# Kernel tuning notes

Hardware: AMD Instinct MI355X
Metric: run time of the kernel (lower is better)

## Reference

```python
import jax, jax.numpy as jnp
import numpy as np

B, T, D, H = 4, 2048, 512, 8
K = D // H  # head dim = 64

def setup_inputs() -> dict:
    key = jax.random.key(0)
    k1, k2, k3, k4 = jax.random.split(key, 4)
    x = jax.random.normal(k1, (B, T, D), dtype=jnp.float32)
    # torch nn.Linear stores weight as [out_features, in_features]
    w_qkv = jax.random.normal(k2, (3 * D, D), dtype=jnp.float32) * (D ** -0.5)
    w_proj = jax.random.normal(k3, (D, D), dtype=jnp.float32) * (D ** -0.5)
    b_proj = jax.random.normal(k4, (D,), dtype=jnp.float32) * 0.01
    return {"x": x, "w_qkv": w_qkv, "w_proj": w_proj, "b_proj": b_proj}

def reference(x, w_qkv, w_proj, b_proj):
    Bx, Tx, Dx = x.shape
    # qkv projection (no bias): [B,T,3D]
    qkv = jnp.einsum('btd,ed->bte', x, w_qkv)
    q, k, v = jnp.split(qkv, 3, axis=-1)
    # [B,H,T,K]
    def heads(t):
        return t.reshape(Bx, Tx, H, K).transpose(0, 2, 1, 3)
    q, k, v = heads(q), heads(k), heads(v)
    # scaled scores with causal mask
    scores = jnp.einsum('bhqk,bhsk->bhqs', q, k) * (K ** -0.5)  # [B,H,T,T]
    causal = jnp.tril(jnp.ones((Tx, Tx), dtype=bool))
    scores = jnp.where(causal, scores, -jnp.inf)
    attn = jax.nn.softmax(scores, axis=-1)  # dropout p=0.0 -> identity
    out = jnp.einsum('bhqs,bhsk->bhqk', attn, v)  # [B,H,T,K]
    out = out.transpose(0, 2, 1, 3).reshape(Bx, Tx, Dx)
    out = jnp.einsum('btd,ed->bte', out, w_proj) + b_proj
    return out
```

## Files before the change

kernel.cpp:

```cpp
#include <hip/hip_runtime.h>


typedef unsigned short u16;
typedef __attribute__((ext_vector_type(8))) __bf16 bf16x8;
typedef __attribute__((ext_vector_type(8))) unsigned short u16x8;
typedef __attribute__((ext_vector_type(4))) float f32x4;

#define DEV static __device__ __forceinline__

DEV void async16(const u16* g, u16* l) {
  __builtin_amdgcn_global_load_lds(
      (const __attribute__((address_space(1))) unsigned int*)g,
      (__attribute__((address_space(3))) unsigned int*)l, 16, 0, 0);
}
DEV u16x8 gld8(const u16* p) { return *(const u16x8*)p; }
DEV void lst8(u16* p, u16x8 v) { *(u16x8*)p = v; }
DEV bf16x8 ldsld8(const u16* p) {
  return __builtin_bit_cast(bf16x8, *(const u16x8*)p);
}
DEV f32x4 mfma16(bf16x8 a, bf16x8 b, f32x4 c) {
  return __builtin_amdgcn_mfma_f32_16x16x32_bf16(a, b, c, 0, 0, 0);
}
DEV u16 f2b(float f) {
  unsigned u = __builtin_bit_cast(unsigned, f);
  u += 0x7FFFu + ((u >> 16) & 1u);
  return (u16)(u >> 16);
}
DEV u16x8 pack8(f32x4 a, f32x4 b) {
  u16x8 r;
  r[0] = f2b(a[0]); r[1] = f2b(a[1]); r[2] = f2b(a[2]); r[3] = f2b(a[3]);
  r[4] = f2b(b[0]); r[5] = f2b(b[1]); r[6] = f2b(b[2]); r[7] = f2b(b[3]);
  return r;
}

__global__ void cvt_all(const float* __restrict__ x, const float* __restrict__ wq,
                        u16* __restrict__ xb, u16* __restrict__ wqb) {
  constexpr long NX = 8192L * 512 / 8;
  constexpr long NQ = 1536L * 512 / 8;
  const long i = (long)blockIdx.x * 256 + threadIdx.x;
  if (i < NX) {
    const float* p = x + i * 8;
    *(u16x8*)(xb + i * 8) = pack8(*(const f32x4*)p, *(const f32x4*)(p + 4));
  } else if (i < NX + NQ) {
    const long j = i - NX;
    const float* p = wq + j * 8;
    *(u16x8*)(wqb + j * 8) = pack8(*(const f32x4*)p, *(const f32x4*)(p + 4));
  }
}

__global__ void gemm_bb(const u16* __restrict__ A, const u16* __restrict__ Bt,
                        u16* __restrict__ C, int N, int K) {
  __shared__ __align__(16) u16 As[2][128 * 32];
  __shared__ __align__(16) u16 Bs[2][128 * 32];

  const int t = threadIdx.x, lane = t & 63, w = t >> 6;
  const int lane15 = lane & 15, quad = lane >> 4;
  const int wr = w >> 1, wc = w & 1;
  const long row0 = (long)blockIdx.y * 128;
  const int col0 = blockIdx.x * 128;

  const int srow = w * 16 + (lane >> 2);
  const int scol = (lane & 3) * 8;
  const u16* Ag = A + (row0 + srow) * (long)K + scol;
  const u16* Bg = Bt + ((long)col0 + srow) * (long)K + scol;

  f32x4 acc[4][4];
#pragma unroll
  for (int i = 0; i < 4; i++)
#pragma unroll
    for (int j = 0; j < 4; j++) acc[i][j] = (f32x4)(0.0f);

  for (int k0 = 0; k0 < K; k0 += 64) {
    __syncthreads();
#pragma unroll
    for (int r = 0; r < 2; r++) {
#pragma unroll
      for (int hf = 0; hf < 2; hf++) {
        async16(Ag + (long)r * 64 * K + k0 + hf * 32,
                &As[hf][(r * 64 + w * 16) * 32]);
        async16(Bg + (long)r * 64 * K + k0 + hf * 32,
                &Bs[hf][(r * 64 + w * 16) * 32]);
      }
    }
    __syncthreads();

#pragma unroll
    for (int hf = 0; hf < 2; hf++) {
      bf16x8 a[4], b[4];
#pragma unroll
      for (int i = 0; i < 4; i++)
        a[i] = ldsld8(&As[hf][(wr * 64 + i * 16 + lane15) * 32 + quad * 8]);
#pragma unroll
      for (int j = 0; j < 4; j++)
        b[j] = ldsld8(&Bs[hf][(wc * 64 + j * 16 + lane15) * 32 + quad * 8]);
#pragma unroll
      for (int i = 0; i < 4; i++)
#pragma unroll
        for (int j = 0; j < 4; j++) acc[i][j] = mfma16(a[i], b[j], acc[i][j]);
    }
  }

#pragma unroll
  for (int i = 0; i < 4; i++)
#pragma unroll
    for (int j = 0; j < 4; j++) {
      const int col = col0 + wc * 64 + j * 16 + lane15;
#pragma unroll
      for (int r = 0; r < 4; r++) {
        const long row = row0 + wr * 64 + i * 16 + quad * 4 + r;
        C[row * (long)N + col] = f2b(acc[i][j][r]);
      }
    }
}

__global__ void gemm_b64(const u16* __restrict__ A, const float* __restrict__ Bt,
                         const float* __restrict__ bias, float* __restrict__ C,
                         int N, int K) {
  __shared__ __align__(16) u16 As[2][128 * 32];
  __shared__ __align__(16) u16 Bs[2][64 * 32];

  const int t = threadIdx.x, lane = t & 63, w = t >> 6;
  const int lane15 = lane & 15, quad = lane >> 4;
  const int wr = w >> 1, wc = w & 1;
  const long row0 = (long)blockIdx.y * 128;
  const int col0 = blockIdx.x * 64;

  const int srow = w * 16 + (lane >> 2);
  const int scol = (lane & 3) * 8;
  const u16* Ag = A + (row0 + srow) * (long)K + scol;

  const int brow = t >> 2, bc = (t & 3) * 16;
  const float* Bg = Bt + (long)(col0 + brow) * K + bc;
  u16* BsD = &Bs[bc >> 5][brow * 32 + (bc & 31)];

  f32x4 acc[4][2];
#pragma unroll
  for (int i = 0; i < 4; i++)
#pragma unroll
    for (int j = 0; j < 2; j++) acc[i][j] = (f32x4)(0.0f);

  f32x4 q0 = *(const f32x4*)Bg, q1 = *(const f32x4*)(Bg + 4);
  f32x4 q2 = *(const f32x4*)(Bg + 8), q3 = *(const f32x4*)(Bg + 12);

  for (int k0 = 0; k0 < K; k0 += 64) {
    __syncthreads();
#pragma unroll
    for (int r = 0; r < 2; r++)
#pragma unroll
      for (int hf = 0; hf < 2; hf++)
        async16(Ag + (long)r * 64 * K + k0 + hf * 32,
                &As[hf][(r * 64 + w * 16) * 32]);
    lst8(BsD, pack8(q0, q1));
    lst8(BsD + 8, pack8(q2, q3));
    __syncthreads();

    {
      const int kp = (k0 + 64 < K) ? k0 + 64 : k0;
      q0 = *(const f32x4*)(Bg + kp);     q1 = *(const f32x4*)(Bg + kp + 4);
      q2 = *(const f32x4*)(Bg + kp + 8); q3 = *(const f32x4*)(Bg + kp + 12);
    }

#pragma unroll
    for (int hf = 0; hf < 2; hf++) {
      bf16x8 a[4], b[2];
#pragma unroll
      for (int i = 0; i < 4; i++)
        a[i] = ldsld8(&As[hf][(wr * 64 + i * 16 + lane15) * 32 + quad * 8]);
#pragma unroll
      for (int j = 0; j < 2; j++)
        b[j] = ldsld8(&Bs[hf][(wc * 32 + j * 16 + lane15) * 32 + quad * 8]);
#pragma unroll
      for (int i = 0; i < 4; i++)
#pragma unroll
        for (int j = 0; j < 2; j++) acc[i][j] = mfma16(a[i], b[j], acc[i][j]);
    }
  }

#pragma unroll
  for (int i = 0; i < 4; i++)
#pragma unroll
    for (int j = 0; j < 2; j++) {
      const int col = col0 + wc * 32 + j * 16 + lane15;
      const float bv = bias[col];
#pragma unroll
      for (int r = 0; r < 4; r++) {
        const long row = row0 + wr * 64 + i * 16 + quad * 4 + r;
        C[row * (long)N + col] = acc[i][j][r] + bv;
      }
    }
}

__global__ void attn_v3(const u16* __restrict__ qkv, u16* __restrict__ out) {
  constexpr int T = 2048, LD = 1536;
  constexpr float CEXP = 0.18033688f;
  __shared__ __align__(16) u16 Ks[64 * 72];
  __shared__ __align__(16) u16 Vt[64 * 72];
  __shared__ __align__(16) u16 Ps[4][16 * 72];

  const int t = threadIdx.x, lane = t & 63, w = t >> 6;
  const int lane15 = lane & 15, quad = lane >> 4;

  const int i = blockIdx.x;
  int qb = i & 31;
  if (i >= 512) qb = 31 - qb;
  const int h = (i >> 5) & 7;
  const int b = (i >> 8) & 3;
  const long base = (long)b * T * LD;

  const u16* gq =
      qkv + base + (long)(qb * 64 + w * 16 + lane15) * LD + h * 64 + quad * 8;
  const bf16x8 qa0 = __builtin_bit_cast(bf16x8, *(const u16x8*)gq);
  const bf16x8 qa1 = __builtin_bit_cast(bf16x8, *(const u16x8*)(gq + 32));

  const int srow = t >> 3, sc8 = (t & 7) * 8;
  const int vs = t >> 2, vd0 = (t & 3) * 16;

  const int nsb = qb + 1;

  u16x8 kr0, kr1, vr0, vr1;
  {
    const u16* gk = qkv + base + (long)srow * LD + 512 + h * 64 + sc8;
    const u16* gv = qkv + base + (long)vs * LD + 1024 + h * 64 + vd0;
    kr0 = gld8(gk); kr1 = gld8(gk + (long)32 * LD);
    vr0 = gld8(gv); vr1 = gld8(gv + 8);
  }

  float lp[4] = {0.0f, 0.0f, 0.0f, 0.0f};
  f32x4 o[4];
#pragma unroll
  for (int j = 0; j < 4; j++) o[j] = (f32x4)(0.0f);

  const int qrow_base = qb * 64 + w * 16 + quad * 4;

  for (int sb = 0; sb < nsb; ++sb) {
    __syncthreads();
    lst8(&Ks[srow * 72 + sc8], kr0);
    lst8(&Ks[(srow + 32) * 72 + sc8], kr1);
#pragma unroll
    for (int ii = 0; ii < 8; ii++) {
      const int d = vd0 + ii;
      Vt[d * 72 + (vs ^ (((d >> 3) & 7) << 3))] = vr0[ii];
    }
#pragma unroll
    for (int ii = 0; ii < 8; ii++) {
      const int d = vd0 + 8 + ii;
      Vt[d * 72 + (vs ^ (((d >> 3) & 7) << 3))] = vr1[ii];
    }
    __syncthreads();

    {
      const int sp = (sb + 1 < nsb) ? sb + 1 : sb;
      const u16* gk = qkv + base + (long)(sp * 64 + srow) * LD + 512 + h * 64 + sc8;
      const u16* gv = qkv + base + (long)(sp * 64 + vs) * LD + 1024 + h * 64 + vd0;
      kr0 = gld8(gk); kr1 = gld8(gk + (long)32 * LD);
      vr0 = gld8(gv); vr1 = gld8(gv + 8);
    }

    f32x4 sf[4];
#pragma unroll
    for (int j = 0; j < 4; j++) {
      f32x4 z = (f32x4)(0.0f);
      z = mfma16(qa0, ldsld8(&Ks[(j * 16 + lane15) * 72 + quad * 8]), z);
      sf[j] = mfma16(qa1, ldsld8(&Ks[(j * 16 + lane15) * 72 + quad * 8 + 32]), z);
    }

    if (sb == qb) {
      const int scol_base = sb * 64 + lane15;
#pragma unroll
      for (int j = 0; j < 4; j++)
#pragma unroll
        for (int r = 0; r < 4; r++) {
          float p = exp2f(sf[j][r] * CEXP);
          if (scol_base + j * 16 > qrow_base + r) p = 0.0f;
          sf[j][r] = p;
          lp[r] += p;
        }
    } else {
#pragma unroll
      for (int j = 0; j < 4; j++)
#pragma unroll
        for (int r = 0; r < 4; r++) {
          const float p = exp2f(sf[j][r] * CEXP);
          sf[j][r] = p;
          lp[r] += p;
        }
    }

    u16* myP = Ps[w];
#pragma unroll
    for (int j = 0; j < 4; j++)
#pragma unroll
      for (int r = 0; r < 4; r++)
        myP[(quad * 4 + r) * 72 + j * 16 + lane15] = f2b(sf[j][r]);
    __asm__ __volatile__("" ::: "memory");
    const bf16x8 pa0 = ldsld8(&myP[lane15 * 72 + quad * 8]);
    const bf16x8 pa1 = ldsld8(&myP[lane15 * 72 + quad * 8 + 32]);
    __asm__ __volatile__("" ::: "memory");

#pragma unroll
    for (int j = 0; j < 4; j++) {
      const int d0 = j * 16 + lane15;
      const int swz = ((d0 >> 3) & 7) << 3;
      o[j] = mfma16(pa0, ldsld8(&Vt[d0 * 72 + ((quad * 8) ^ swz)]), o[j]);
      o[j] = mfma16(pa1, ldsld8(&Vt[d0 * 72 + ((quad * 8 + 32) ^ swz)]), o[j]);
    }
  }

#pragma unroll
  for (int off = 1; off < 16; off <<= 1)
#pragma unroll
    for (int r = 0; r < 4; r++) lp[r] += __shfl_xor(lp[r], off);

  const long orow0 = (long)b * T + qb * 64 + w * 16;
  float inv[4];
#pragma unroll
  for (int r = 0; r < 4; r++) inv[r] = 1.0f / lp[r];
#pragma unroll
  for (int j = 0; j < 4; j++)
#pragma unroll
    for (int r = 0; r < 4; r++)
      out[(orow0 + quad * 4 + r) * 512 + h * 64 + j * 16 + lane15] =
          f2b(o[j][r] * inv[r]);
}

extern "C" void kernel_launch(void* const* d_in, const int* in_sizes, int n_in,
                              void* d_out, int out_size, void* d_ws, size_t ws_size,
                              hipStream_t stream) {
  const float* x      = (const float*)d_in[0];
  const float* w_qkv  = (const float*)d_in[1];
  const float* w_proj = (const float*)d_in[2];
  const float* b_proj = (const float*)d_in[3];
  float* out = (float*)d_out;

  u16* qkv = (u16*)d_ws;
  u16* xb  = qkv + (size_t)8192 * 1536;
  u16* wqb = (u16*)d_out;

  cvt_all<<<2432, 256, 0, stream>>>(x, w_qkv, xb, wqb);
  gemm_bb<<<dim3(12, 64), 256, 0, stream>>>(xb, wqb, qkv, 1536, 512);
  attn_v3<<<1024, 256, 0, stream>>>(qkv, xb);
  gemm_b64<<<dim3(8, 64), 256, 0, stream>>>(xb, w_proj, b_proj, out, 512, 512);
}
```

Baseline: 163.8 us.

## Fuse fp32-to-bf16 conversion into QKV GEMM and enlarge attention query tiles

Removes the separate conversion kernel: the QKV GEMM now loads fp32 x and weights, packs them to bf16 in registers and stores to LDS, with register prefetch of the next K tile instead of async global-to-LDS loads. The attention kernel moves to 512-thread blocks covering 128 query rows (8 waves) sharing each K/V tile, which halves K/V loads per query, and waves skip key blocks that lie fully above their causal range. Bf16 packing switches to the HIP intrinsic conversion. The costs are more fp32 global traffic inside the GEMM, synchronous loads in place of the async path, and idle waves at block barriers on the diagonal.

```diff
diff --git a/kernel.cpp b/kernel.cpp
--- a/kernel.cpp
+++ b/kernel.cpp
@@ -1,10 +1,12 @@
 #include <hip/hip_runtime.h>
+#include <hip/hip_bf16.h>
 
 
 typedef unsigned short u16;
 typedef __attribute__((ext_vector_type(8))) __bf16 bf16x8;
 typedef __attribute__((ext_vector_type(8))) unsigned short u16x8;
 typedef __attribute__((ext_vector_type(4))) float f32x4;
+typedef __attribute__((ext_vector_type(4))) unsigned u32x4;
 
 #define DEV static __device__ __forceinline__
 
@@ -26,30 +28,23 @@
   u += 0x7FFFu + ((u >> 16) & 1u);
   return (u16)(u >> 16);
 }
+DEV unsigned pk2(float x, float y) {
+  __hip_bfloat162 t = __float22bfloat162_rn(float2{x, y});
+  unsigned r;
+  __builtin_memcpy(&r, &t, 4);
+  return r;
+}
 DEV u16x8 pack8(f32x4 a, f32x4 b) {
-  u16x8 r;
-  r[0] = f2b(a[0]); r[1] = f2b(a[1]); r[2] = f2b(a[2]); r[3] = f2b(a[3]);
-  r[4] = f2b(b[0]); r[5] = f2b(b[1]); r[6] = f2b(b[2]); r[7] = f2b(b[3]);
-  return r;
-}
-
-__global__ void cvt_all(const float* __restrict__ x, const float* __restrict__ wq,
-                        u16* __restrict__ xb, u16* __restrict__ wqb) {
-  constexpr long NX = 8192L * 512 / 8;
-  constexpr long NQ = 1536L * 512 / 8;
-  const long i = (long)blockIdx.x * 256 + threadIdx.x;
-  if (i < NX) {
-    const float* p = x + i * 8;
-    *(u16x8*)(xb + i * 8) = pack8(*(const f32x4*)p, *(const f32x4*)(p + 4));
-  } else if (i < NX + NQ) {
-    const long j = i - NX;
-    const float* p = wq + j * 8;
-    *(u16x8*)(wqb + j * 8) = pack8(*(const f32x4*)p, *(const f32x4*)(p + 4));
-  }
-}
-
-__global__ void gemm_bb(const u16* __restrict__ A, const u16* __restrict__ Bt,
-                        u16* __restrict__ C, int N, int K) {
+  u32x4 t;
+  t[0] = pk2(a[0], a[1]);
+  t[1] = pk2(a[2], a[3]);
+  t[2] = pk2(b[0], b[1]);
+  t[3] = pk2(b[2], b[3]);
+  return __builtin_bit_cast(u16x8, t);
+}
+
+__global__ void gemm1f(const float* __restrict__ A, const float* __restrict__ Bt,
+                       u16* __restrict__ C, int N, int K) {
   __shared__ __align__(16) u16 As[2][128 * 32];
   __shared__ __align__(16) u16 Bs[2][128 * 32];
 
@@ -59,10 +54,18 @@
   const long row0 = (long)blockIdx.y * 128;
   const int col0 = blockIdx.x * 128;
 
-  const int srow = w * 16 + (lane >> 2);
-  const int scol = (lane & 3) * 8;
-  const u16* Ag = A + (row0 + srow) * (long)K + scol;
-  const u16* Bg = Bt + ((long)col0 + srow) * (long)K + scol;
+  const int sr = t >> 2, sc = (t & 3) * 8;
+  const float* Ag = A + (row0 + sr) * (long)K + sc;
+  const float* Bg = Bt + (long)(col0 + sr) * K + sc;
+  u16* AsD[2][2];
+  u16* BsD[2][2];
+#pragma unroll
+  for (int r = 0; r < 2; r++)
+#pragma unroll
+    for (int hf = 0; hf < 2; hf++) {
+      AsD[r][hf] = &As[hf][(sr + r * 64) * 32 + sc];
+      BsD[r][hf] = &Bs[hf][(sr + r * 64) * 32 + sc];
+    }
 
   f32x4 acc[4][4];
 #pragma unroll
@@ -70,19 +73,40 @@
 #pragma unroll
     for (int j = 0; j < 4; j++) acc[i][j] = (f32x4)(0.0f);
 
+  u16x8 ra[2][2], rb[2][2];
+#pragma unroll
+  for (int r = 0; r < 2; r++)
+#pragma unroll
+    for (int hf = 0; hf < 2; hf++) {
+      const float* pa = Ag + (long)r * 64 * K + hf * 32;
+      const float* pb = Bg + (long)r * 64 * K + hf * 32;
+      ra[r][hf] = pack8(*(const f32x4*)pa, *(const f32x4*)(pa + 4));
+      rb[r][hf] = pack8(*(const f32x4*)pb, *(const f32x4*)(pb + 4));
+    }
+
   for (int k0 = 0; k0 < K; k0 += 64) {
     __syncthreads();
 #pragma unroll
-    for (int r = 0; r < 2; r++) {
+    for (int r = 0; r < 2; r++)
 #pragma unroll
       for (int hf = 0; hf < 2; hf++) {
-        async16(Ag + (long)r * 64 * K + k0 + hf * 32,
-                &As[hf][(r * 64 + w * 16) * 32]);
-        async16(Bg + (long)r * 64 * K + k0 + hf * 32,
-                &Bs[hf][(r * 64 + w * 16) * 32]);
+        lst8(AsD[r][hf], ra[r][hf]);
+        lst8(BsD[r][hf], rb[r][hf]);
       }
-    }
-    __syncthreads();
+    __syncthreads();
+
+    {
+      const int kp = (k0 + 64 < K) ? k0 + 64 : k0;
+#pragma unroll
+      for (int r = 0; r < 2; r++)
+#pragma unroll
+        for (int hf = 0; hf < 2; hf++) {
+          const float* pa = Ag + (long)r * 64 * K + kp + hf * 32;
+          const float* pb = Bg + (long)r * 64 * K + kp + hf * 32;
+          ra[r][hf] = pack8(*(const f32x4*)pa, *(const f32x4*)(pa + 4));
+          rb[r][hf] = pack8(*(const f32x4*)pb, *(const f32x4*)(pb + 4));
+        }
+    }
 
 #pragma unroll
     for (int hf = 0; hf < 2; hf++) {
@@ -190,39 +214,39 @@
     }
 }
 
-__global__ void attn_v3(const u16* __restrict__ qkv, u16* __restrict__ out) {
+__global__ void attn_v4(const u16* __restrict__ qkv, u16* __restrict__ out) {
   constexpr int T = 2048, LD = 1536;
   constexpr float CEXP = 0.18033688f;
   __shared__ __align__(16) u16 Ks[64 * 72];
   __shared__ __align__(16) u16 Vt[64 * 72];
-  __shared__ __align__(16) u16 Ps[4][16 * 72];
+  __shared__ __align__(16) u16 Ps[8][16 * 72];
 
   const int t = threadIdx.x, lane = t & 63, w = t >> 6;
   const int lane15 = lane & 15, quad = lane >> 4;
 
   const int i = blockIdx.x;
-  int qb = i & 31;
-  if (i >= 512) qb = 31 - qb;
-  const int h = (i >> 5) & 7;
-  const int b = (i >> 8) & 3;
+  int qt = i & 15;
+  if (i >= 256) qt = 15 - qt;
+  const int h = (i >> 4) & 7;
+  const int b = (i >> 7) & 3;
   const long base = (long)b * T * LD;
 
   const u16* gq =
-      qkv + base + (long)(qb * 64 + w * 16 + lane15) * LD + h * 64 + quad * 8;
+      qkv + base + (long)(qt * 128 + w * 16 + lane15) * LD + h * 64 + quad * 8;
   const bf16x8 qa0 = __builtin_bit_cast(bf16x8, *(const u16x8*)gq);
   const bf16x8 qa1 = __builtin_bit_cast(bf16x8, *(const u16x8*)(gq + 32));
 
   const int srow = t >> 3, sc8 = (t & 7) * 8;
-  const int vs = t >> 2, vd0 = (t & 3) * 16;
-
-  const int nsb = qb + 1;
-
-  u16x8 kr0, kr1, vr0, vr1;
+  const int vs = t >> 3, vd0 = (t & 7) * 8;
+
+  const int nsb = 2 * qt + 2;
+
+  u16x8 kr, vr;
   {
     const u16* gk = qkv + base + (long)srow * LD + 512 + h * 64 + sc8;
     const u16* gv = qkv + base + (long)vs * LD + 1024 + h * 64 + vd0;
-    kr0 = gld8(gk); kr1 = gld8(gk + (long)32 * LD);
-    vr0 = gld8(gv); vr1 = gld8(gv + 8);
+    kr = gld8(gk);
+    vr = gld8(gv);
   }
 
   float lp[4] = {0.0f, 0.0f, 0.0f, 0.0f};
@@ -230,21 +254,16 @@
 #pragma unroll
   for (int j = 0; j < 4; j++) o[j] = (f32x4)(0.0f);
 
-  const int qrow_base = qb * 64 + w * 16 + quad * 4;
+  const int qrow_base = qt * 128 + w * 16 + quad * 4;
+  const int qrow_wave_max = qt * 128 + w * 16 + 15;
 
   for (int sb = 0; sb < nsb; ++sb) {
     __syncthreads();
-    lst8(&Ks[srow * 72 + sc8], kr0);
-    lst8(&Ks[(srow + 32) * 72 + sc8], kr1);
+    lst8(&Ks[srow * 72 + sc8], kr);
 #pragma unroll
     for (int ii = 0; ii < 8; ii++) {
       const int d = vd0 + ii;
-      Vt[d * 72 + (vs ^ (((d >> 3) & 7) << 3))] = vr0[ii];
-    }
-#pragma unroll
-    for (int ii = 0; ii < 8; ii++) {
-      const int d = vd0 + 8 + ii;
-      Vt[d * 72 + (vs ^ (((d >> 3) & 7) << 3))] = vr1[ii];
+      Vt[d * 72 + (vs ^ (((d >> 3) & 7) << 3))] = vr[ii];
     }
     __syncthreads();
 
@@ -252,9 +271,11 @@
       const int sp = (sb + 1 < nsb) ? sb + 1 : sb;
       const u16* gk = qkv + base + (long)(sp * 64 + srow) * LD + 512 + h * 64 + sc8;
       const u16* gv = qkv + base + (long)(sp * 64 + vs) * LD + 1024 + h * 64 + vd0;
-      kr0 = gld8(gk); kr1 = gld8(gk + (long)32 * LD);
-      vr0 = gld8(gv); vr1 = gld8(gv + 8);
-    }
+      kr = gld8(gk);
+      vr = gld8(gv);
+    }
+
+    if (sb * 64 > qrow_wave_max) continue;
 
     f32x4 sf[4];
 #pragma unroll
@@ -264,7 +285,7 @@
       sf[j] = mfma16(qa1, ldsld8(&Ks[(j * 16 + lane15) * 72 + quad * 8 + 32]), z);
     }
 
-    if (sb == qb) {
+    if (sb >= 2 * qt) {
       const int scol_base = sb * 64 + lane15;
 #pragma unroll
       for (int j = 0; j < 4; j++)
@@ -311,7 +332,7 @@
 #pragma unroll
     for (int r = 0; r < 4; r++) lp[r] += __shfl_xor(lp[r], off);
 
-  const long orow0 = (long)b * T + qb * 64 + w * 16;
+  const long orow0 = (long)b * T + qt * 128 + w * 16;
   float inv[4];
 #pragma unroll
   for (int r = 0; r < 4; r++) inv[r] = 1.0f / lp[r];
@@ -332,12 +353,10 @@
   const float* b_proj = (const float*)d_in[3];
   float* out = (float*)d_out;
 
-  u16* qkv = (u16*)d_ws;
-  u16* xb  = qkv + (size_t)8192 * 1536;
-  u16* wqb = (u16*)d_out;
-
-  cvt_all<<<2432, 256, 0, stream>>>(x, w_qkv, xb, wqb);
-  gemm_bb<<<dim3(12, 64), 256, 0, stream>>>(xb, wqb, qkv, 1536, 512);
-  attn_v3<<<1024, 256, 0, stream>>>(qkv, xb);
-  gemm_b64<<<dim3(8, 64), 256, 0, stream>>>(xb, w_proj, b_proj, out, 512, 512);
-}
+  u16* qkv  = (u16*)d_ws;
+  u16* attn = qkv + (size_t)8192 * 1536;
+
+  gemm1f<<<dim3(12, 64), 256, 0, stream>>>(x, w_qkv, qkv, 1536, 512);
+  attn_v4<<<512, 512, 0, stream>>>(qkv, attn);
+  gemm_b64<<<dim3(8, 64), 256, 0, stream>>>(attn, w_proj, b_proj, out, 512, 512);
+}
```

After: 232.8 us. +42.1%, slower.

## Process two query sub-tiles per attention block to share K/V staging

Applied to the files above, without the earlier changes.

The attention kernel now handles 128 query rows per block, split into two 64-row sub-tiles, so each K/V tile staged into LDS serves both. This halves the number of blocks and the global K/V reads, with heavy tiles scheduled first. The softmax scale is folded into the Q columns in the QKV GEMM epilogue, which removes a multiply inside the exp loop. The bf16 packing now uses the packed HIP conversion intrinsic. In exchange, each block holds more registers and the grid is half as large, which may lower occupancy and load balance.

```diff
diff --git a/kernel.cpp b/kernel.cpp
--- a/kernel.cpp
+++ b/kernel.cpp
@@ -1,10 +1,12 @@
 #include <hip/hip_runtime.h>
+#include <hip/hip_bf16.h>
 
 
 typedef unsigned short u16;
 typedef __attribute__((ext_vector_type(8))) __bf16 bf16x8;
 typedef __attribute__((ext_vector_type(8))) unsigned short u16x8;
 typedef __attribute__((ext_vector_type(4))) float f32x4;
+typedef __attribute__((ext_vector_type(4))) unsigned u32x4;
 
 #define DEV static __device__ __forceinline__
 
@@ -26,11 +28,19 @@
   u += 0x7FFFu + ((u >> 16) & 1u);
   return (u16)(u >> 16);
 }
+DEV unsigned pk2(float x, float y) {
+  __hip_bfloat162 t = __float22bfloat162_rn(float2{x, y});
+  unsigned r;
+  __builtin_memcpy(&r, &t, 4);
+  return r;
+}
 DEV u16x8 pack8(f32x4 a, f32x4 b) {
-  u16x8 r;
-  r[0] = f2b(a[0]); r[1] = f2b(a[1]); r[2] = f2b(a[2]); r[3] = f2b(a[3]);
-  r[4] = f2b(b[0]); r[5] = f2b(b[1]); r[6] = f2b(b[2]); r[7] = f2b(b[3]);
-  return r;
+  u32x4 t;
+  t[0] = pk2(a[0], a[1]);
+  t[1] = pk2(a[2], a[3]);
+  t[2] = pk2(b[0], b[1]);
+  t[3] = pk2(b[2], b[3]);
+  return __builtin_bit_cast(u16x8, t);
 }
 
 __global__ void cvt_all(const float* __restrict__ x, const float* __restrict__ wq,
@@ -73,7 +83,7 @@
   for (int k0 = 0; k0 < K; k0 += 64) {
     __syncthreads();
 #pragma unroll
-    for (int r = 0; r < 2; r++) {
+    for (int r = 0; r < 2; r++)
 #pragma unroll
       for (int hf = 0; hf < 2; hf++) {
         async16(Ag + (long)r * 64 * K + k0 + hf * 32,
@@ -81,7 +91,6 @@
         async16(Bg + (long)r * 64 * K + k0 + hf * 32,
                 &Bs[hf][(r * 64 + w * 16) * 32]);
       }
-    }
     __syncthreads();
 
 #pragma unroll
@@ -105,10 +114,11 @@
 #pragma unroll
     for (int j = 0; j < 4; j++) {
       const int col = col0 + wc * 64 + j * 16 + lane15;
+      const float sc = (col < 512) ? 0.18033688f : 1.0f;
 #pragma unroll
       for (int r = 0; r < 4; r++) {
         const long row = row0 + wr * 64 + i * 16 + quad * 4 + r;
-        C[row * (long)N + col] = f2b(acc[i][j][r]);
+        C[row * (long)N + col] = f2b(acc[i][j][r] * sc);
       }
     }
 }
@@ -190,32 +200,34 @@
     }
 }
 
-__global__ void attn_v3(const u16* __restrict__ qkv, u16* __restrict__ out) {
+__global__ void attn_v5(const u16* __restrict__ qkv, u16* __restrict__ out) {
   constexpr int T = 2048, LD = 1536;
-  constexpr float CEXP = 0.18033688f;
   __shared__ __align__(16) u16 Ks[64 * 72];
   __shared__ __align__(16) u16 Vt[64 * 72];
-  __shared__ __align__(16) u16 Ps[4][16 * 72];
+  __shared__ __align__(16) u16 Ps[4][2][16 * 72];
 
   const int t = threadIdx.x, lane = t & 63, w = t >> 6;
   const int lane15 = lane & 15, quad = lane >> 4;
 
-  const int i = blockIdx.x;
-  int qb = i & 31;
-  if (i >= 512) qb = 31 - qb;
-  const int h = (i >> 5) & 7;
-  const int b = (i >> 8) & 3;
+  const int bx = blockIdx.x;
+  const int qt = 15 - (bx >> 5);
+  const int h = bx & 7, b = (bx >> 3) & 3;
   const long base = (long)b * T * LD;
 
-  const u16* gq =
-      qkv + base + (long)(qb * 64 + w * 16 + lane15) * LD + h * 64 + quad * 8;
-  const bf16x8 qa0 = __builtin_bit_cast(bf16x8, *(const u16x8*)gq);
-  const bf16x8 qa1 = __builtin_bit_cast(bf16x8, *(const u16x8*)(gq + 32));
+  bf16x8 qa[2][2];
+#pragma unroll
+  for (int sp = 0; sp < 2; sp++) {
+    const u16* gq = qkv + base +
+                    (long)(qt * 128 + sp * 64 + w * 16 + lane15) * LD +
+                    h * 64 + quad * 8;
+    qa[sp][0] = __builtin_bit_cast(bf16x8, *(const u16x8*)gq);
+    qa[sp][1] = __builtin_bit_cast(bf16x8, *(const u16x8*)(gq + 32));
+  }
 
   const int srow = t >> 3, sc8 = (t & 7) * 8;
   const int vs = t >> 2, vd0 = (t & 3) * 16;
 
-  const int nsb = qb + 1;
+  const int nsb = 2 * qt + 2;
 
   u16x8 kr0, kr1, vr0, vr1;
   {
@@ -225,12 +237,12 @@
     vr0 = gld8(gv); vr1 = gld8(gv + 8);
   }
 
-  float lp[4] = {0.0f, 0.0f, 0.0f, 0.0f};
-  f32x4 o[4];
-#pragma unroll
-  for (int j = 0; j < 4; j++) o[j] = (f32x4)(0.0f);
-
-  const int qrow_base = qb * 64 + w * 16 + quad * 4;
+  float lp[2][4] = {{0, 0, 0, 0}, {0, 0, 0, 0}};
+  f32x4 o[2][4];
+#pragma unroll
+  for (int sp = 0; sp < 2; sp++)
+#pragma unroll
+    for (int j = 0; j < 4; j++) o[sp][j] = (f32x4)(0.0f);
 
   for (int sb = 0; sb < nsb; ++sb) {
     __syncthreads();
@@ -249,78 +261,91 @@
     __syncthreads();
 
     {
-      const int sp = (sb + 1 < nsb) ? sb + 1 : sb;
-      const u16* gk = qkv + base + (long)(sp * 64 + srow) * LD + 512 + h * 64 + sc8;
-      const u16* gv = qkv + base + (long)(sp * 64 + vs) * LD + 1024 + h * 64 + vd0;
+      const int nx = (sb + 1 < nsb) ? sb + 1 : sb;
+      const u16* gk = qkv + base + (long)(nx * 64 + srow) * LD + 512 + h * 64 + sc8;
+      const u16* gv = qkv + base + (long)(nx * 64 + vs) * LD + 1024 + h * 64 + vd0;
       kr0 = gld8(gk); kr1 = gld8(gk + (long)32 * LD);
       vr0 = gld8(gv); vr1 = gld8(gv + 8);
     }
 
-    f32x4 sf[4];
-#pragma unroll
-    for (int j = 0; j < 4; j++) {
-      f32x4 z = (f32x4)(0.0f);
-      z = mfma16(qa0, ldsld8(&Ks[(j * 16 + lane15) * 72 + quad * 8]), z);
-      sf[j] = mfma16(qa1, ldsld8(&Ks[(j * 16 + lane15) * 72 + quad * 8 + 32]), z);
-    }
-
-    if (sb == qb) {
-      const int scol_base = sb * 64 + lane15;
+#pragma unroll
+    for (int sp = 0; sp < 2; sp++) {
+      if (sb > 2 * qt + sp) continue;
+
+      f32x4 sf[4];
+#pragma unroll
+      for (int j = 0; j < 4; j++) {
+        f32x4 z = (f32x4)(0.0f);
+        z = mfma16(qa[sp][0], ldsld8(&Ks[(j * 16 + lane15) * 72 + quad * 8]), z);
+        sf[j] = mfma16(qa[sp][1],
+                       ldsld8(&Ks[(j * 16 + lane15) * 72 + quad * 8 + 32]), z);
+      }
+
+      if (sb == 2 * qt + sp) {
+        const int qrow_base = qt * 128 + sp * 64 + w * 16 + quad * 4;
+        const int scol_base = sb * 64 + lane15;
+#pragma unroll
+        for (int j = 0; j < 4; j++)
+#pragma unroll
+          for (int r = 0; r < 4; r++) {
+            float p = exp2f(sf[j][r]);
+            if (scol_base + j * 16 > qrow_base + r) p = 0.0f;
+            sf[j][r] = p;
+            lp[sp][r] += p;
+          }
+      } else {
+#pragma unroll
+        for (int j = 0; j < 4; j++)
+#pragma unroll
+          for (int r = 0; r < 4; r++) {
+            const float p = exp2f(sf[j][r]);
+            sf[j][r] = p;
+            lp[sp][r] += p;
+          }
+      }
+
+      u16* myP = Ps[w][sp];
 #pragma unroll
       for (int j = 0; j < 4; j++)
 #pragma unroll
-        for (int r = 0; r < 4; r++) {
-          float p = exp2f(sf[j][r] * CEXP);
-          if (scol_base + j * 16 > qrow_base + r) p = 0.0f;
-          sf[j][r] = p;
-          lp[r] += p;
-        }
-    } else {
-#pragma unroll
-      for (int j = 0; j < 4; j++)
-#pragma unroll
-        for (int r = 0; r < 4; r++) {
-          const float p = exp2f(sf[j][r] * CEXP);
-          sf[j][r] = p;
-          lp[r] += p;
-        }
-    }
-
-    u16* myP = Ps[w];
+        for (int r = 0; r < 4; r++)
+          myP[(quad * 4 + r) * 72 + j * 16 + lane15] = f2b(sf[j][r]);
+      __asm__ __volatile__("" ::: "memory");
+      const bf16x8 pa0 = ldsld8(&myP[lane15 * 72 + quad * 8]);
+      const bf16x8 pa1 = ldsld8(&myP[lane15 * 72 + quad * 8 + 32]);
+      __asm__ __volatile__("" ::: "memory");
+
+#pragma unroll
+      for (int j = 0; j < 4; j++) {
+        const int d0 = j * 16 + lane15;
+        const int swz = ((d0 >> 3) & 7) << 3;
+        o[sp][j] = mfma16(pa0, ldsld8(&Vt[d0 * 72 + ((quad * 8) ^ swz)]), o[sp][j]);
+        o[sp][j] =
+            mfma16(pa1, ldsld8(&Vt[d0 * 72 + ((quad * 8 + 32) ^ swz)]), o[sp][j]);
+      }
+    }
+  }
+
+#pragma unroll
+  for (int off = 1; off < 16; off <<= 1)
+#pragma unroll
+    for (int sp = 0; sp < 2; sp++)
+#pragma unroll
+      for (int r = 0; r < 4; r++) lp[sp][r] += __shfl_xor(lp[sp][r], off);
+
+#pragma unroll
+  for (int sp = 0; sp < 2; sp++) {
+    const long orow0 = (long)b * T + qt * 128 + sp * 64 + w * 16;
+    float inv[4];
+#pragma unroll
+    for (int r = 0; r < 4; r++) inv[r] = 1.0f / lp[sp][r];
 #pragma unroll
     for (int j = 0; j < 4; j++)
 #pragma unroll
       for (int r = 0; r < 4; r++)
-        myP[(quad * 4 + r) * 72 + j * 16 + lane15] = f2b(sf[j][r]);
-    __asm__ __volatile__("" ::: "memory");
-    const bf16x8 pa0 = ldsld8(&myP[lane15 * 72 + quad * 8]);
-    const bf16x8 pa1 = ldsld8(&myP[lane15 * 72 + quad * 8 + 32]);
-    __asm__ __volatile__("" ::: "memory");
-
-#pragma unroll
-    for (int j = 0; j < 4; j++) {
-      const int d0 = j * 16 + lane15;
-      const int swz = ((d0 >> 3) & 7) << 3;
-      o[j] = mfma16(pa0, ldsld8(&Vt[d0 * 72 + ((quad * 8) ^ swz)]), o[j]);
-      o[j] = mfma16(pa1, ldsld8(&Vt[d0 * 72 + ((quad * 8 + 32) ^ swz)]), o[j]);
-    }
-  }
-
-#pragma unroll
-  for (int off = 1; off < 16; off <<= 1)
-#pragma unroll
-    for (int r = 0; r < 4; r++) lp[r] += __shfl_xor(lp[r], off);
-
-  const long orow0 = (long)b * T + qb * 64 + w * 16;
-  float inv[4];
-#pragma unroll
-  for (int r = 0; r < 4; r++) inv[r] = 1.0f / lp[r];
-#pragma unroll
-  for (int j = 0; j < 4; j++)
-#pragma unroll
-    for (int r = 0; r < 4; r++)
-      out[(orow0 + quad * 4 + r) * 512 + h * 64 + j * 16 + lane15] =
-          f2b(o[j][r] * inv[r]);
+        out[(orow0 + quad * 4 + r) * 512 + h * 64 + j * 16 + lane15] =
+            f2b(o[sp][j][r] * inv[r]);
+  }
 }
 
 extern "C" void kernel_launch(void* const* d_in, const int* in_sizes, int n_in,
@@ -338,6 +363,6 @@
 
   cvt_all<<<2432, 256, 0, stream>>>(x, w_qkv, xb, wqb);
   gemm_bb<<<dim3(12, 64), 256, 0, stream>>>(xb, wqb, qkv, 1536, 512);
-  attn_v3<<<1024, 256, 0, stream>>>(qkv, xb);
+  attn_v5<<<512, 256, 0, stream>>>(qkv, xb);
   gemm_b64<<<dim3(8, 64), 256, 0, stream>>>(xb, w_proj, b_proj, out, 512, 512);
 }
```

After: 259.6 us. 1.59x slower.
